# Kernel tuning notes

Hardware: AMD Instinct MI355X
Metric: run time of the kernel (lower is better)

Reference implementation:

```python
import jax, jax.numpy as jnp
import numpy as np
from jax import lax

MARGIN = 0.5
EPS = 1e-12


def _l2norm(x, axis=-1):
    n = jnp.sqrt(jnp.sum(x * x, axis=axis, keepdims=True))
    return x / jnp.maximum(n, EPS)


def setup_inputs() -> dict:
    key = jax.random.key(0)
    ks = jax.random.split(key, 18)
    B, T, N, Din = 1, 8, 4096, 128
    hid = 256
    D = 2 * hid  # out_dim = 2*hidden_dim[-1]
    Tp, Ttr, M, K = 4, 5, 2048, 16
    s = 0.05
    return {
        "x_feature": jax.random.normal(ks[0], (B, Ttr, N, 1), jnp.float32),
        "x_graph": jax.random.normal(ks[1], (B, T, N, Din), jnp.float32),
        "x_graph_inv": jax.random.normal(ks[2], (B, T, N, Din), jnp.float32),
        "temp_y": jax.random.randint(ks[3], (Tp, M, 2 + K), 0, N),
        "is_leaf": jax.random.uniform(ks[4], (Tp, N), dtype=jnp.float32),
        "W_gcn": jax.random.normal(ks[5], (Din, hid), jnp.float32) * s,
        "b_gcn": jnp.zeros((hid,), jnp.float32),
        "Wx_zr": jax.random.normal(ks[6], (D, 2 * D), jnp.float32) * s,
        "Wh_zr": jax.random.normal(ks[7], (D, 2 * D), jnp.float32) * s,
        "b_zr": jnp.zeros((2 * D,), jnp.float32),
        "Wx_c": jax.random.normal(ks[8], (D, D), jnp.float32) * s,
        "Wh_c": jax.random.normal(ks[9], (D, D), jnp.float32) * s,
        "b_c": jnp.zeros((D,), jnp.float32),
        "h_vecs": jax.random.normal(ks[10], (Tp, D), jnp.float32),
        "W_leaf": jax.random.normal(ks[11], (D, 1), jnp.float32) * s,
        "b_leaf": jnp.zeros((1,), jnp.float32),
        "W_conv": jax.random.normal(ks[12], (Ttr, Tp), jnp.float32) * s,
        "b_conv": jnp.zeros((Tp,), jnp.float32),
        "cur_node_num": N,
    }


def reference(x_feature, x_graph, x_graph_inv, temp_y, is_leaf,
              W_gcn, b_gcn, Wx_zr, Wh_zr, b_zr, Wx_c, Wh_c, b_c,
              h_vecs, W_leaf, b_leaf, W_conv, b_conv, cur_node_num):
    B = x_graph.shape[0]
    N_all = x_graph.shape[2]
    # t_gcn on both graph views, concat -> [B,T,N,D]
    h = jax.nn.relu(jnp.einsum('btnd,dh->btnh', x_graph, W_gcn) + b_gcn)
    h_inv = jax.nn.relu(jnp.einsum('btnd,dh->btnh', x_graph_inv, W_gcn) + b_gcn)
    h_final = jnp.concatenate((h, h_inv), axis=-1)
    D = h_final.shape[-1]

    # sequential GRU (TGCNCell) over time_span via scan
    def cell(hs, x):
        zr = jax.nn.sigmoid(x @ Wx_zr + hs @ Wh_zr + b_zr)
        z, r = jnp.split(zr, 2, axis=-1)
        c = jnp.tanh(x @ Wx_c + (r * hs) @ Wh_c + b_c)
        return z * hs + (1.0 - z) * c, None

    h0 = jnp.zeros((B, N_all, D), h_final.dtype)
    hT, _ = lax.scan(cell, h0, jnp.moveaxis(h_final, 1, 0))
    h_trans = _l2norm(hT.reshape(-1, D)[:cur_node_num])  # [N,D]

    # grid predictions (t_conv surrogate): [B,Ttr,N,1] -> [Tp, B*N] -> [Tp,N]
    feat = x_feature[..., 0].transpose(0, 2, 1)            # [B,N,Ttr]
    g = feat @ W_conv + b_conv                             # [B,N,Tp]
    grid_x = jnp.moveaxis(g, 2, 0).reshape(g.shape[-1], -1)[:, :cur_node_num]

    # Householder reflections per predicted step
    hn = _l2norm(h_vecs)                                   # [Tp,D]
    W_trans = jnp.eye(D, dtype=hn.dtype) - 2.0 * hn[:, :, None] * hn[:, None, :]

    leaf_logits = jax.nn.sigmoid(h_trans @ W_leaf + b_leaf)  # [N,1]
    lvec = leaf_logits[:, 0]

    def per_t(W_t, idx_t, yleaf_t, grid_t):
        pos = h_trans[idx_t[:, 1]]            # [M,D]
        neg = h_trans[idx_t[:, 2:]]           # [M,K,D]
        a = pos @ W_t                          # [M,D]
        score_neg = 1.0 - jnp.einsum('md,mkd->mk', a, neg)
        score_pos = 1.0 - jnp.sum(a * pos, axis=-1, keepdims=True)
        loss_off = jnp.mean(jax.nn.relu(score_pos - score_neg + MARGIN))
        # BCEWithLogits applied to sigmoid outputs (faithful to source)
        loss_leaf = jnp.mean(jnp.maximum(lvec, 0.0) - lvec * yleaf_t + jnp.log1p(jnp.exp(-jnp.abs(lvec))))
        h_s = h_trans @ W_t                    # [N,D]
        score_all = h_s @ h_s.T                # [N,N]
        final = lvec * grid_t                  # [N]
        att = score_all @ final                # [N]
        return att, loss_off, loss_leaf

    att_pre, lo, ll = jax.vmap(per_t)(W_trans, temp_y, is_leaf, grid_x)
    return att_pre, jnp.mean(lo), jnp.mean(ll)
```

## Files before the change

kernel.cpp:

```cpp
#include <hip/hip_runtime.h>
#include <hip/hip_bf16.h>
#include <hip/hip_fp16.h>
#include <math.h>

typedef __hip_bfloat16 bf16;
typedef __attribute__((ext_vector_type(8))) short short8;
typedef __attribute__((ext_vector_type(4))) float f32x4;

union UB { short8 v; bf16 e[8]; };
union UH { short8 v; __half e[8]; };

__device__ __forceinline__ float wred(float v) {
  #pragma unroll
  for (int o = 32; o > 0; o >>= 1) v += __shfl_xor(v, o, 64);
  return v;
}
__device__ __forceinline__ float sigf(float x) { return 1.f / (1.f + expf(-x)); }

__device__ __forceinline__ void gl_lds16(const bf16* g, const bf16* lds) {
  __builtin_amdgcn_global_load_lds((const __attribute__((address_space(1))) void*)g,
                                   (__attribute__((address_space(3))) void*)lds,
                                   16, 0, 0);
}
__device__ __forceinline__ f32x4 mfma16(short8 a, short8 b, f32x4 c) {
  return __builtin_amdgcn_mfma_f32_16x16x32_bf16(a, b, c, 0, 0, 0);
}

__global__ __launch_bounds__(256, 2)
void gemmx(const bf16* __restrict__ A, const bf16* __restrict__ Wxzrt,
           const bf16* __restrict__ Wxct, const float* __restrict__ b_zr,
           const float* __restrict__ b_c, bf16* __restrict__ xzrp,
           bf16* __restrict__ xcp)
{
  __shared__ __align__(16) char smem[34816];
  bf16* As = (bf16*)smem;
  bf16* Bs = (bf16*)(smem + 16384);
  __half* Ts = (__half*)smem;

  const int tid  = threadIdx.x;
  const int wave = tid >> 6, lane = tid & 63;
  const int lm = lane & 15, q = lane >> 4;
  const int brow = blockIdx.x, bcol = blockIdx.y;
  const int wr = (wave >> 1) * 64, wc = (wave & 1) * 64;
  const int srow = lane >> 3, sslot = lane & 7;

  const bf16* Bt; const float* bias; bf16* C; int ldc, colbase;
  if (bcol < 8) { Bt = Wxzrt + (size_t)bcol * 128 * 512; bias = b_zr; C = xzrp; ldc = 1024; colbase = bcol * 128; }
  else          { Bt = Wxct + (size_t)(bcol - 8) * 128 * 512; bias = b_c; C = xcp; ldc = 512; colbase = (bcol - 8) * 128; }

  f32x4 acc[4][4];
  #pragma unroll
  for (int i = 0; i < 4; ++i)
    #pragma unroll
    for (int j = 0; j < 4; ++j) acc[i][j] = (f32x4){0.f, 0.f, 0.f, 0.f};

  for (int kb = 0; kb < 512; kb += 64) {
    #pragma unroll
    for (int j = 0; j < 4; ++j) {
      int ml = wave * 32 + j * 8 + srow;
      int cg = sslot ^ (ml & 7);
      gl_lds16(A + (size_t)(brow * 128 + ml) * 512 + kb + cg * 8, As + (wave * 4 + j) * 512);
      gl_lds16(Bt + (size_t)ml * 512 + kb + cg * 8, Bs + (wave * 4 + j) * 512);
    }
    __syncthreads();
    #pragma unroll
    for (int ks = 0; ks < 2; ++ks) {
      short8 af[4], bfr[4];
      #pragma unroll
      for (int i = 0; i < 4; ++i) {
        int cg = ks * 4 + q;
        int ml = wr + i * 16 + lm;
        af[i]  = *(const short8*)(As + ml * 64 + ((cg ^ (ml & 7)) * 8));
        int nl = wc + i * 16 + lm;
        bfr[i] = *(const short8*)(Bs + nl * 64 + ((cg ^ (nl & 7)) * 8));
      }
      #pragma unroll
      for (int i = 0; i < 4; ++i)
        #pragma unroll
        for (int j = 0; j < 4; ++j)
          acc[i][j] = mfma16(af[i], bfr[j], acc[i][j]);
    }
    __syncthreads();
  }
  #pragma unroll
  for (int i = 0; i < 4; ++i)
    #pragma unroll
    for (int j = 0; j < 4; ++j) {
      int col = wc + j * 16 + lm;
      float bv = bias[colbase + col];
      #pragma unroll
      for (int p = 0; p < 4; ++p)
        Ts[(wr + i * 16 + q * 4 + p) * 136 + col] = __float2half(acc[i][j][p] + bv);
    }
  __syncthreads();
  int rg = tid >> 4, cl = tid & 15;
  #pragma unroll
  for (int v = 0; v < 8; ++v) {
    int row = v * 16 + rg;
    UH t; t.v = *(const short8*)(Ts + row * 136 + cl * 8);
    UB o;
    #pragma unroll
    for (int e = 0; e < 8; ++e) o.e[e] = __float2bfloat16(__half2float(t.e[e]));
    *(short8*)(C + (size_t)(brow * 128 + row) * ldc + colbase + cl * 8) = o.v;
  }
}

__global__ __launch_bounds__(256, 2)
void gcnk(const float* __restrict__ Ag, const float* __restrict__ Agi,
          const bf16* __restrict__ Wgt, const float* __restrict__ bias,
          bf16* __restrict__ out)
{
  __shared__ __align__(16) char smem[34816];
  bf16* As = (bf16*)smem;
  bf16* Bs = (bf16*)(smem + 16384);
  __half* Ts = (__half*)smem;

  const int tid  = threadIdx.x;
  const int wave = tid >> 6, lane = tid & 63;
  const int lm = lane & 15, q = lane >> 4;
  const int brow = blockIdx.x, bcol = blockIdx.y;
  const int z = blockIdx.z, cout = z * 256;
  const float* A = z ? Agi : Ag;
  const int wr = (wave >> 1) * 64, wc = (wave & 1) * 64;
  const int srow = lane >> 3, sslot = lane & 7;

  f32x4 acc[4][4];
  #pragma unroll
  for (int i = 0; i < 4; ++i)
    #pragma unroll
    for (int j = 0; j < 4; ++j) acc[i][j] = (f32x4){0.f, 0.f, 0.f, 0.f};

  for (int kb = 0; kb < 128; kb += 64) {
    #pragma unroll
    for (int j = 0; j < 4; ++j) {
      int ml = wave * 32 + j * 8 + srow;
      int cg = sslot ^ (ml & 7);
      const float* src = A + (size_t)(brow * 128 + ml) * 128 + kb + cg * 8;
      bf16 tmp[8];
      #pragma unroll
      for (int e = 0; e < 8; ++e) tmp[e] = __float2bfloat16(src[e]);
      *(short8*)(As + ml * 64 + sslot * 8) = *(const short8*)tmp;
      gl_lds16(Wgt + (size_t)(bcol * 128 + ml) * 128 + kb + cg * 8,
               Bs + (wave * 4 + j) * 512);
    }
    __syncthreads();
    #pragma unroll
    for (int ks = 0; ks < 2; ++ks) {
      short8 af[4], bfr[4];
      #pragma unroll
      for (int i = 0; i < 4; ++i) {
        int cg = ks * 4 + q;
        int ml = wr + i * 16 + lm;
        af[i]  = *(const short8*)(As + ml * 64 + ((cg ^ (ml & 7)) * 8));
        int nl = wc + i * 16 + lm;
        bfr[i] = *(const short8*)(Bs + nl * 64 + ((cg ^ (nl & 7)) * 8));
      }
      #pragma unroll
      for (int i = 0; i < 4; ++i)
        #pragma unroll
        for (int j = 0; j < 4; ++j)
          acc[i][j] = mfma16(af[i], bfr[j], acc[i][j]);
    }
    __syncthreads();
  }
  #pragma unroll
  for (int i = 0; i < 4; ++i)
    #pragma unroll
    for (int j = 0; j < 4; ++j) {
      int col = wc + j * 16 + lm;
      float bv = bias[bcol * 128 + col];
      #pragma unroll
      for (int p = 0; p < 4; ++p)
        Ts[(wr + i * 16 + q * 4 + p) * 136 + col] = __float2half(acc[i][j][p] + bv);
    }
  __syncthreads();
  int rg = tid >> 4, cl = tid & 15;
  #pragma unroll
  for (int v = 0; v < 8; ++v) {
    int row = v * 16 + rg;
    UH t; t.v = *(const short8*)(Ts + row * 136 + cl * 8);
    UB o;
    #pragma unroll
    for (int e = 0; e < 8; ++e) o.e[e] = __float2bfloat16(fmaxf(__half2float(t.e[e]), 0.f));
    *(short8*)(out + (size_t)(brow * 128 + row) * 512 + cout + bcol * 128 + cl * 8) = o.v;
  }
}

__global__ __launch_bounds__(512, 2)
void gruz(const bf16* __restrict__ hsb, const bf16* __restrict__ Wzr,
          const bf16* __restrict__ xz, __half* __restrict__ zh,
          bf16* __restrict__ rhb, int t0)
{
  __shared__ __align__(16) bf16 As[64 * 512];
  __half* Ts = (__half*)As;

  const int tid  = threadIdx.x;
  const int w    = tid >> 6, lane = tid & 63;
  const int lm   = lane & 15, q = lane >> 4;
  const int g    = blockIdx.x, s = blockIdx.y;
  const int grow = g * 64;

  const int prow = tid >> 3, pc0 = (tid & 7) * 32;
  const size_t gr = (size_t)(grow + prow);
  UB xv[4], h8[4];
  #pragma unroll
  for (int j = 0; j < 4; ++j)
    xv[j].v = *(const short8*)(xz + gr * 1024 + s * 256 + pc0 + j * 8);
  if (s >= 2 && !t0) {
    #pragma unroll
    for (int j = 0; j < 4; ++j)
      h8[j].v = *(const short8*)(hsb + gr * 512 + (s - 2) * 256 + pc0 + j * 8);
  }

  f32x4 acc[4][2];
  #pragma unroll
  for (int mf = 0; mf < 4; ++mf)
    #pragma unroll
    for (int nf = 0; nf < 2; ++nf) acc[mf][nf] = (f32x4){0.f, 0.f, 0.f, 0.f};

  if (!t0) {
    #pragma unroll
    for (int j = 0; j < 8; ++j) {
      int row = w * 8 + j;
      gl_lds16(hsb + (size_t)(grow + row) * 512 + ((lane ^ (row & 7)) * 8),
               As + row * 512);
    }
    __syncthreads();

    const bf16* Bp = Wzr + (size_t)(s * 16 + w * 2) * 8192 + lane * 8;
    short8 b0[2], b1[2], a[4];
    #pragma unroll
    for (int nf = 0; nf < 2; ++nf) {
      b0[nf] = *(const short8*)(Bp + (size_t)nf * 8192);
      b1[nf] = *(const short8*)(Bp + (size_t)nf * 8192 + 512);
    }
    #pragma unroll
    for (int mf = 0; mf < 4; ++mf) {
      int row = mf * 16 + lm;
      a[mf] = *(const short8*)(As + row * 512 + ((q ^ (row & 7)) * 8));
    }
    #pragma unroll
    for (int KS = 0; KS < 16; ++KS) {
      short8 bn[2], an[4];
      if (KS < 14) {
        #pragma unroll
        for (int nf = 0; nf < 2; ++nf)
          bn[nf] = *(const short8*)(Bp + (size_t)nf * 8192 + (KS + 2) * 512);
      }
      if (KS < 15) {
        #pragma unroll
        for (int mf = 0; mf < 4; ++mf) {
          int row = mf * 16 + lm;
          an[mf] = *(const short8*)(As + row * 512 + ((((KS + 1) * 4 + q) ^ (row & 7)) * 8));
        }
      }
      #pragma unroll
      for (int nf = 0; nf < 2; ++nf)
        #pragma unroll
        for (int mf = 0; mf < 4; ++mf)
          acc[mf][nf] = mfma16(a[mf], b0[nf], acc[mf][nf]);
      #pragma unroll
      for (int nf = 0; nf < 2; ++nf) { b0[nf] = b1[nf]; b1[nf] = bn[nf]; }
      #pragma unroll
      for (int mf = 0; mf < 4; ++mf) a[mf] = an[mf];
    }
    __syncthreads();
  }

  #pragma unroll
  for (int mf = 0; mf < 4; ++mf)
    #pragma unroll
    for (int nf = 0; nf < 2; ++nf)
      #pragma unroll
      for (int p = 0; p < 4; ++p)
        Ts[(mf * 16 + q * 4 + p) * 264 + w * 32 + nf * 16 + lm] =
          __float2half(acc[mf][nf][p]);
  __syncthreads();

  #pragma unroll
  for (int j = 0; j < 4; ++j) {
    int c = pc0 + j * 8;
    UH tv; tv.v = *(const short8*)(Ts + prow * 264 + c);
    if (s < 2) {
      UH o;
      #pragma unroll
      for (int e = 0; e < 8; ++e)
        o.e[e] = __float2half(sigf(__half2float(tv.e[e]) + (float)xv[j].e[e]));
      *(short8*)(zh + gr * 512 + s * 256 + c) = o.v;
    } else if (!t0) {
      UB o;
      #pragma unroll
      for (int e = 0; e < 8; ++e) {
        float r = sigf(__half2float(tv.e[e]) + (float)xv[j].e[e]);
        o.e[e] = __float2bfloat16(r * (float)h8[j].e[e]);
      }
      *(short8*)(rhb + gr * 512 + (s - 2) * 256 + c) = o.v;
    }
  }
}

__global__ __launch_bounds__(512, 2)
void gruc(const bf16* __restrict__ rhb, const bf16* __restrict__ Wc,
          const bf16* __restrict__ xc, const __half* __restrict__ zh,
          bf16* __restrict__ hsb, int t0)
{
  __shared__ __align__(16) bf16 As[64 * 512];
  __half* Ts = (__half*)As;

  const int tid  = threadIdx.x;
  const int w    = tid >> 6, lane = tid & 63;
  const int lm   = lane & 15, q = lane >> 4;
  const int rh_  = w & 1, cq = w >> 1;
  const int g    = blockIdx.x, s = blockIdx.y;
  const int grow = g * 64;

  const int prow = tid >> 3, pc0 = (tid & 7) * 16;
  const size_t gr = (size_t)(grow + prow);
  UB xv[2], h8[2]; UH zv[2];
  #pragma unroll
  for (int j = 0; j < 2; ++j) {
    int hc = s * 128 + pc0 + j * 8;
    xv[j].v = *(const short8*)(xc + gr * 512 + hc);
    zv[j].v = *(const short8*)(zh + gr * 512 + hc);
  }
  if (!t0) {
    #pragma unroll
    for (int j = 0; j < 2; ++j)
      h8[j].v = *(const short8*)(hsb + gr * 512 + s * 128 + pc0 + j * 8);
  }

  f32x4 acc[2][2];
  #pragma unroll
  for (int mf = 0; mf < 2; ++mf)
    #pragma unroll
    for (int nf = 0; nf < 2; ++nf) acc[mf][nf] = (f32x4){0.f, 0.f, 0.f, 0.f};

  if (!t0) {
    #pragma unroll
    for (int j = 0; j < 8; ++j) {
      int row = w * 8 + j;
      gl_lds16(rhb + (size_t)(grow + row) * 512 + ((lane ^ (row & 7)) * 8),
               As + row * 512);
    }
    __syncthreads();

    const bf16* Bp = Wc + (size_t)(s * 8 + cq * 2) * 8192 + lane * 8;
    short8 b0[2], b1[2], a[2];
    #pragma unroll
    for (int nf = 0; nf < 2; ++nf) {
      b0[nf] = *(const short8*)(Bp + (size_t)nf * 8192);
      b1[nf] = *(const short8*)(Bp + (size_t)nf * 8192 + 512);
    }
    #pragma unroll
    for (int mf = 0; mf < 2; ++mf) {
      int row = rh_ * 32 + mf * 16 + lm;
      a[mf] = *(const short8*)(As + row * 512 + ((q ^ (row & 7)) * 8));
    }
    #pragma unroll
    for (int KS = 0; KS < 16; ++KS) {
      short8 bn[2], an[2];
      if (KS < 14) {
        #pragma unroll
        for (int nf = 0; nf < 2; ++nf)
          bn[nf] = *(const short8*)(Bp + (size_t)nf * 8192 + (KS + 2) * 512);
      }
      if (KS < 15) {
        #pragma unroll
        for (int mf = 0; mf < 2; ++mf) {
          int row = rh_ * 32 + mf * 16 + lm;
          an[mf] = *(const short8*)(As + row * 512 + ((((KS + 1) * 4 + q) ^ (row & 7)) * 8));
        }
      }
      #pragma unroll
      for (int nf = 0; nf < 2; ++nf)
        #pragma unroll
        for (int mf = 0; mf < 2; ++mf)
          acc[mf][nf] = mfma16(a[mf], b0[nf], acc[mf][nf]);
      #pragma unroll
      for (int nf = 0; nf < 2; ++nf) { b0[nf] = b1[nf]; b1[nf] = bn[nf]; }
      #pragma unroll
      for (int mf = 0; mf < 2; ++mf) a[mf] = an[mf];
    }
    __syncthreads();
  }

  #pragma unroll
  for (int mf = 0; mf < 2; ++mf)
    #pragma unroll
    for (int nf = 0; nf < 2; ++nf)
      #pragma unroll
      for (int p = 0; p < 4; ++p)
        Ts[(rh_ * 32 + mf * 16 + q * 4 + p) * 136 + cq * 32 + nf * 16 + lm] =
          __float2half(acc[mf][nf][p]);
  __syncthreads();

  #pragma unroll
  for (int j = 0; j < 2; ++j) {
    int c = pc0 + j * 8;
    int hc = s * 128 + c;
    UH tv; tv.v = *(const short8*)(Ts + prow * 136 + c);
    UB o;
    #pragma unroll
    for (int e = 0; e < 8; ++e) {
      float cd = tanhf(__half2float(tv.e[e]) + (float)xv[j].e[e]);
      float zc = __half2float(zv[j].e[e]);
      float ho = t0 ? 0.f : (float)h8[j].e[e];
      o.e[e] = __float2bfloat16(zc * ho + (1.f - zc) * cd);
    }
    *(short8*)(hsb + gr * 512 + hc) = o.v;
  }
}

__global__ void prep(const float* __restrict__ Wh_zr, const float* __restrict__ Wh_c,
                     const float* __restrict__ Wx_zr, const float* __restrict__ Wx_c,
                     const float* __restrict__ W_gcn,
                     bf16* __restrict__ Whzrt, bf16* __restrict__ Whct,
                     bf16* __restrict__ Wxzrt, bf16* __restrict__ Wxct,
                     bf16* __restrict__ Wgt) {
  int i = blockIdx.x * 256 + threadIdx.x;
  if (i < 524288) {
    int n = i >> 9, k = i & 511;
    int off = ((n >> 4) * 16 + (k >> 5)) * 512 + ((k >> 3) & 3) * 128 + (n & 15) * 8 + (k & 7);
    Whzrt[off] = __float2bfloat16(Wh_zr[(size_t)k * 1024 + n]);
  } else if (i < 786432) {
    int j = i - 524288; int n = j >> 9, k = j & 511;
    int off = ((n >> 4) * 16 + (k >> 5)) * 512 + ((k >> 3) & 3) * 128 + (n & 15) * 8 + (k & 7);
    Whct[off] = __float2bfloat16(Wh_c[(size_t)k * 512 + n]);
  } else if (i < 1310720) {
    int j = i - 786432; int n = j >> 9, k = j & 511;
    Wxzrt[j] = __float2bfloat16(Wx_zr[(size_t)k * 1024 + n]);
  } else if (i < 1572864) {
    int j = i - 1310720; int n = j >> 9, k = j & 511;
    Wxct[j] = __float2bfloat16(Wx_c[(size_t)k * 512 + n]);
  } else {
    int j = i - 1572864; int n = j >> 7, k = j & 127;
    Wgt[j] = __float2bfloat16(W_gcn[(size_t)k * 256 + n]);
  }
}

__global__ void norm_lvec(const bf16* __restrict__ hsb, const float* __restrict__ Wl,
                          const float* __restrict__ bl, const float* __restrict__ hv,
                          bf16* __restrict__ Htrb, float* __restrict__ lv,
                          float* __restrict__ hn) {
  int w = threadIdx.x >> 6, lane = threadIdx.x & 63;
  if (blockIdx.x == 1024) {
    float x[8], ss = 0.f;
    #pragma unroll
    for (int j = 0; j < 8; ++j) { x[j] = hv[w * 512 + lane * 8 + j]; ss += x[j] * x[j]; }
    ss = wred(ss);
    float inv = 1.f / fmaxf(sqrtf(ss), 1e-12f);
    #pragma unroll
    for (int j = 0; j < 8; ++j) hn[w * 512 + lane * 8 + j] = x[j] * inv;
    return;
  }
  int n = blockIdx.x * 4 + w;
  float x[8], ss = 0.f;
  #pragma unroll
  for (int j = 0; j < 8; ++j) {
    x[j] = (float)hsb[(size_t)n * 512 + lane * 8 + j];
    ss += x[j] * x[j];
  }
  ss = wred(ss);
  float inv = 1.f / fmaxf(sqrtf(ss), 1e-12f);
  float dot = 0.f;
  #pragma unroll
  for (int j = 0; j < 8; ++j) {
    float vv = x[j] * inv;
    Htrb[(size_t)n * 512 + lane * 8 + j] = __float2bfloat16(vv);
    dot += vv * Wl[lane * 8 + j];
  }
  dot = wred(dot);
  if (lane == 0) lv[n] = sigf(dot + bl[0]);
}

__global__ void htf(const bf16* __restrict__ Htrb, const float* __restrict__ xf,
                    const float* __restrict__ Wc, const float* __restrict__ bc,
                    const float* __restrict__ lv, float* __restrict__ v) {
  __shared__ float fin_s[4][64];
  int ch = blockIdx.x;
  int d = threadIdx.x;
  int n0 = ch * 64;
  if (d < 256) {
    int t = d >> 6, i = d & 63, n = n0 + i;
    float g = bc[t];
    #pragma unroll
    for (int tt = 0; tt < 5; ++tt) g += xf[tt * 4096 + n] * Wc[tt * 4 + t];
    fin_s[t][i] = lv[n] * g;
  }
  __syncthreads();
  float s0 = 0.f, s1 = 0.f, s2 = 0.f, s3 = 0.f;
  for (int i = 0; i < 64; ++i) {
    float hv = (float)Htrb[(size_t)(n0 + i) * 512 + d];
    s0 += hv * fin_s[0][i];
    s1 += hv * fin_s[1][i];
    s2 += hv * fin_s[2][i];
    s3 += hv * fin_s[3][i];
  }
  atomicAdd(&v[d], s0);
  atomicAdd(&v[512 + d], s1);
  atomicAdd(&v[1024 + d], s2);
  atomicAdd(&v[1536 + d], s3);
}

__global__ void attk(const bf16* __restrict__ Htrb, const float* __restrict__ v,
                     float* __restrict__ out) {
  int w = threadIdx.x >> 6, lane = threadIdx.x & 63;
  int n = blockIdx.x * 4 + w;
  float x[8];
  #pragma unroll
  for (int j = 0; j < 8; ++j) x[j] = (float)Htrb[(size_t)n * 512 + lane * 8 + j];
  #pragma unroll
  for (int t = 0; t < 4; ++t) {
    float s = 0.f;
    #pragma unroll
    for (int j = 0; j < 8; ++j) s += x[j] * v[t * 512 + lane * 8 + j];
    s = wred(s);
    if (lane == 0) out[t * 4096 + n] = s;
  }
}

__global__ void loff(const bf16* __restrict__ Htrb, const float* __restrict__ hn,
                     const int* __restrict__ ty, float* __restrict__ loffp) {
  int w = threadIdx.x >> 6, lane = threadIdx.x & 63;
  int t = blockIdx.y;
  int m = blockIdx.x * 4 + w;
  const int* row = ty + ((size_t)t * 2048 + m) * 18;
  int pi = row[1];
  float p[8], hv[8], c = 0.f;
  #pragma unroll
  for (int j = 0; j < 8; ++j) {
    p[j]  = (float)Htrb[(size_t)pi * 512 + lane * 8 + j];
    hv[j] = hn[t * 512 + lane * 8 + j];
    c += p[j] * hv[j];
  }
  c = wred(c);
  float a[8], sp = 0.f;
  #pragma unroll
  for (int j = 0; j < 8; ++j) { a[j] = p[j] - 2.f * c * hv[j]; sp += a[j] * p[j]; }
  sp = wred(sp);
  float acc = 0.f;
  for (int k = 0; k < 16; ++k) {
    int ni = row[2 + k];
    float sn = 0.f;
    #pragma unroll
    for (int j = 0; j < 8; ++j) sn += a[j] * (float)Htrb[(size_t)ni * 512 + lane * 8 + j];
    sn = wred(sn);
    acc += fmaxf(sn - sp + 0.5f, 0.f);
  }
  __shared__ float sbuf[4];
  if (lane == 0) sbuf[w] = acc;
  __syncthreads();
  if (threadIdx.x == 0)
    loffp[t * 512 + blockIdx.x] = sbuf[0] + sbuf[1] + sbuf[2] + sbuf[3];
}

__global__ void fini(const float* __restrict__ loffp, const float* __restrict__ lv,
                     const float* __restrict__ yl, float* __restrict__ out) {
  int tid = threadIdx.x, w = tid >> 6, lane = tid & 63;
  float s = 0.f, s2 = 0.f;
  for (int i = tid; i < 2048; i += 256) s += loffp[i];
  for (int i = tid; i < 4096; i += 256) {
    float l = lv[i];
    float ym = 0.25f * (yl[i] + yl[4096 + i] + yl[8192 + i] + yl[12288 + i]);
    s2 += fmaxf(l, 0.f) - l * ym + log1pf(expf(-fabsf(l)));
  }
  s = wred(s); s2 = wred(s2);
  __shared__ float sb[4], sb2[4];
  if (lane == 0) { sb[w] = s; sb2[w] = s2; }
  __syncthreads();
  if (tid == 0) {
    out[16384] = (sb[0] + sb[1] + sb[2] + sb[3]) / (4.f * 2048.f * 16.f);
    out[16385] = (sb2[0] + sb2[1] + sb2[2] + sb2[3]) / 4096.f;
  }
}

__global__ void wsprobe(float marker, float* out) {
  if (threadIdx.x == 0) out[0] = marker;
}

extern "C" void kernel_launch(void* const* d_in, const int* in_sizes, int n_in,
                              void* d_out, int out_size, void* d_ws, size_t ws_size,
                              hipStream_t stream) {
  const float* x_feature   = (const float*)d_in[0];
  const float* x_graph     = (const float*)d_in[1];
  const float* x_graph_inv = (const float*)d_in[2];
  const int*   temp_y      = (const int*)d_in[3];
  const float* is_leaf     = (const float*)d_in[4];
  const float* W_gcn       = (const float*)d_in[5];
  const float* b_gcn       = (const float*)d_in[6];
  const float* Wx_zr       = (const float*)d_in[7];
  const float* Wh_zr       = (const float*)d_in[8];
  const float* b_zr        = (const float*)d_in[9];
  const float* Wx_c        = (const float*)d_in[10];
  const float* Wh_c        = (const float*)d_in[11];
  const float* b_c         = (const float*)d_in[12];
  const float* h_vecs      = (const float*)d_in[13];
  const float* W_leaf      = (const float*)d_in[14];
  const float* b_leaf      = (const float*)d_in[15];
  const float* W_conv      = (const float*)d_in[16];
  const float* b_conv      = (const float*)d_in[17];
  float* out = (float*)d_out;
  (void)in_sizes; (void)n_in; (void)out_size;

  const size_t NEED = 156000000;
  if (ws_size < NEED) {
    wsprobe<<<1, 64, 0, stream>>>(1000.f + (float)(ws_size >> 20), out);
    return;
  }

  char* ws = (char*)d_ws;
  size_t off = 0;
  auto alloc = [&](size_t bytes) -> void* {
    void* p = ws + off;
    off = (off + bytes + 255) & ~(size_t)255;
    return p;
  };
  bf16*   Whzrt = (bf16*)  alloc((size_t)1024 * 512 * 2);
  bf16*   Whct  = (bf16*)  alloc((size_t)512 * 512 * 2);
  bf16*   Wxzrt = (bf16*)  alloc((size_t)1024 * 512 * 2);
  bf16*   Wxct  = (bf16*)  alloc((size_t)512 * 512 * 2);
  bf16*   Wgt   = (bf16*)  alloc((size_t)256 * 128 * 2);
  bf16*   hfin  = (bf16*)  alloc((size_t)32768 * 512 * 2);
  bf16*   xzrp  = (bf16*)  alloc((size_t)32768 * 1024 * 2);
  bf16*   xcp   = (bf16*)  alloc((size_t)32768 * 512 * 2);
  bf16*   hsb   = (bf16*)  alloc((size_t)4096 * 512 * 2);
  bf16*   rhb   = (bf16*)  alloc((size_t)4096 * 512 * 2);
  __half* zh    = (__half*)alloc((size_t)4096 * 512 * 2);
  float*  lv    = (float*) alloc(4096 * 4);
  float*  hn    = (float*) alloc(4 * 512 * 4);
  float*  v     = (float*) alloc(4 * 512 * 4);
  float*  loffp = (float*) alloc(2048 * 4);
  bf16*   Htrb  = hfin;

  hipMemsetAsync(v, 0, 4 * 512 * 4, stream);

  prep<<<6272, 256, 0, stream>>>(Wh_zr, Wh_c, Wx_zr, Wx_c, W_gcn,
                                 Whzrt, Whct, Wxzrt, Wxct, Wgt);
  gcnk<<<dim3(256, 2, 2), 256, 0, stream>>>(x_graph, x_graph_inv, Wgt, b_gcn, hfin);
  gemmx<<<dim3(256, 12), 256, 0, stream>>>(hfin, Wxzrt, Wxct, b_zr, b_c, xzrp, xcp);

  for (int t = 0; t < 8; ++t) {
    gruz<<<dim3(64, 4), 512, 0, stream>>>(hsb, Whzrt,
                                          xzrp + (size_t)t * 4096 * 1024,
                                          zh, rhb, t == 0);
    gruc<<<dim3(64, 4), 512, 0, stream>>>(rhb, Whct,
                                          xcp + (size_t)t * 4096 * 512,
                                          zh, hsb, t == 0);
  }

  norm_lvec<<<1025, 256, 0, stream>>>(hsb, W_leaf, b_leaf, h_vecs, Htrb, lv, hn);
  htf<<<64, 512, 0, stream>>>(Htrb, x_feature, W_conv, b_conv, lv, v);
  attk<<<1024, 256, 0, stream>>>(Htrb, v, out);
  loff<<<dim3(512, 4), 256, 0, stream>>>(Htrb, hn, temp_y, loffp);
  fini<<<1, 256, 0, stream>>>(loffp, lv, is_leaf, out);
}
```

Before: 423.8 us.

## Fuse GRU time loop into one persistent kernel with per-group spin barriers

Replaces the 16 separate gruz/gruc launches across 8 timesteps with a single persistent kernel of 256 blocks. Groups of 4 blocks that share a 64-row slice synchronise through atomic counters in global memory, and hsb/rhb are loaded with a cache-coherent flag. This removes launch overhead and the device-wide kernel boundaries between recurrent steps. The cost is that correctness depends on all 256 blocks being resident at once, which is needed to avoid deadlock, and the spin-waiting adds its own overhead.

```diff
diff --git a/kernel.cpp b/kernel.cpp
--- a/kernel.cpp
+++ b/kernel.cpp
@@ -22,8 +22,27 @@
                                    (__attribute__((address_space(3))) void*)lds,
                                    16, 0, 0);
 }
+__device__ __forceinline__ void gl_lds16c(const bf16* g, const bf16* lds) {
+  __builtin_amdgcn_global_load_lds((const __attribute__((address_space(1))) void*)g,
+                                   (__attribute__((address_space(3))) void*)lds,
+                                   16, 0, 1);
+}
 __device__ __forceinline__ f32x4 mfma16(short8 a, short8 b, f32x4 c) {
   return __builtin_amdgcn_mfma_f32_16x16x32_bf16(a, b, c, 0, 0, 0);
+}
+
+__device__ __forceinline__ void gang_sync(unsigned* f) {
+  __syncthreads();
+  if (threadIdx.x == 0) {
+    __hip_atomic_fetch_add(f, 1u, __ATOMIC_RELEASE, __HIP_MEMORY_SCOPE_AGENT);
+    int it = 0;
+    while (__hip_atomic_load(f, __ATOMIC_RELAXED, __HIP_MEMORY_SCOPE_AGENT) < 4u) {
+      __builtin_amdgcn_s_sleep(2);
+      if (++it > (1 << 27)) break;
+    }
+    (void)__hip_atomic_load(f, __ATOMIC_ACQUIRE, __HIP_MEMORY_SCOPE_AGENT);
+  }
+  __syncthreads();
 }
 
 __global__ __launch_bounds__(256, 2)
@@ -187,9 +206,10 @@
 }
 
 __global__ __launch_bounds__(512, 2)
-void gruz(const bf16* __restrict__ hsb, const bf16* __restrict__ Wzr,
-          const bf16* __restrict__ xz, __half* __restrict__ zh,
-          bf16* __restrict__ rhb, int t0)
+void grup(const bf16* __restrict__ Wzr, const bf16* __restrict__ Wc,
+          const bf16* __restrict__ xzrp, const bf16* __restrict__ xcp,
+          __half* __restrict__ zh, bf16* __restrict__ rhb,
+          bf16* __restrict__ hsb, unsigned* __restrict__ flags)
 {
   __shared__ __align__(16) bf16 As[64 * 512];
   __half* Ts = (__half*)As;
@@ -197,217 +217,217 @@
   const int tid  = threadIdx.x;
   const int w    = tid >> 6, lane = tid & 63;
   const int lm   = lane & 15, q = lane >> 4;
-  const int g    = blockIdx.x, s = blockIdx.y;
+  const int bid  = blockIdx.x;
+  const int s    = (bid >> 3) & 3;
+  const int g    = ((bid >> 5) << 3) | (bid & 7);
   const int grow = g * 64;
-
-  const int prow = tid >> 3, pc0 = (tid & 7) * 32;
+  const int rh_  = w & 1, cq = w >> 1;
+  const int prow = tid >> 3;
   const size_t gr = (size_t)(grow + prow);
-  UB xv[4], h8[4];
-  #pragma unroll
-  for (int j = 0; j < 4; ++j)
-    xv[j].v = *(const short8*)(xz + gr * 1024 + s * 256 + pc0 + j * 8);
-  if (s >= 2 && !t0) {
-    #pragma unroll
-    for (int j = 0; j < 4; ++j)
-      h8[j].v = *(const short8*)(hsb + gr * 512 + (s - 2) * 256 + pc0 + j * 8);
-  }
-
-  f32x4 acc[4][2];
-  #pragma unroll
-  for (int mf = 0; mf < 4; ++mf)
-    #pragma unroll
-    for (int nf = 0; nf < 2; ++nf) acc[mf][nf] = (f32x4){0.f, 0.f, 0.f, 0.f};
-
-  if (!t0) {
-    #pragma unroll
-    for (int j = 0; j < 8; ++j) {
-      int row = w * 8 + j;
-      gl_lds16(hsb + (size_t)(grow + row) * 512 + ((lane ^ (row & 7)) * 8),
-               As + row * 512);
-    }
-    __syncthreads();
-
-    const bf16* Bp = Wzr + (size_t)(s * 16 + w * 2) * 8192 + lane * 8;
-    short8 b0[2], b1[2], a[4];
-    #pragma unroll
-    for (int nf = 0; nf < 2; ++nf) {
-      b0[nf] = *(const short8*)(Bp + (size_t)nf * 8192);
-      b1[nf] = *(const short8*)(Bp + (size_t)nf * 8192 + 512);
-    }
-    #pragma unroll
-    for (int mf = 0; mf < 4; ++mf) {
-      int row = mf * 16 + lm;
-      a[mf] = *(const short8*)(As + row * 512 + ((q ^ (row & 7)) * 8));
-    }
-    #pragma unroll
-    for (int KS = 0; KS < 16; ++KS) {
-      short8 bn[2], an[4];
-      if (KS < 14) {
-        #pragma unroll
-        for (int nf = 0; nf < 2; ++nf)
-          bn[nf] = *(const short8*)(Bp + (size_t)nf * 8192 + (KS + 2) * 512);
-      }
-      if (KS < 15) {
+  const int pc1 = (tid & 7) * 32;
+  const int pc2 = (tid & 7) * 16;
+  unsigned* gf = flags + g * 16;
+
+  for (int t = 0; t < 8; ++t) {
+    const bool t0 = (t == 0);
+    const bf16* xz = xzrp + (size_t)t * 4096 * 1024;
+    const bf16* xc = xcp  + (size_t)t * 4096 * 512;
+
+    {
+      UB xv[4], h8[4];
+      #pragma unroll
+      for (int j = 0; j < 4; ++j)
+        xv[j].v = *(const short8*)(xz + gr * 1024 + s * 256 + pc1 + j * 8);
+      if (s >= 2 && !t0) {
+        #pragma unroll
+        for (int j = 0; j < 4; ++j)
+          h8[j].v = *(const short8*)(hsb + gr * 512 + (s - 2) * 256 + pc1 + j * 8);
+      }
+
+      f32x4 acc[4][2];
+      #pragma unroll
+      for (int mf = 0; mf < 4; ++mf)
+        #pragma unroll
+        for (int nf = 0; nf < 2; ++nf) acc[mf][nf] = (f32x4){0.f, 0.f, 0.f, 0.f};
+
+      if (!t0) {
+        #pragma unroll
+        for (int j = 0; j < 8; ++j) {
+          int row = w * 8 + j;
+          gl_lds16c(hsb + (size_t)(grow + row) * 512 + ((lane ^ (row & 7)) * 8),
+                    As + row * 512);
+        }
+        __syncthreads();
+
+        const bf16* Bp = Wzr + (size_t)(s * 16 + w * 2) * 8192 + lane * 8;
+        short8 b0[2], b1[2], a[4];
+        #pragma unroll
+        for (int nf = 0; nf < 2; ++nf) {
+          b0[nf] = *(const short8*)(Bp + (size_t)nf * 8192);
+          b1[nf] = *(const short8*)(Bp + (size_t)nf * 8192 + 512);
+        }
         #pragma unroll
         for (int mf = 0; mf < 4; ++mf) {
           int row = mf * 16 + lm;
-          an[mf] = *(const short8*)(As + row * 512 + ((((KS + 1) * 4 + q) ^ (row & 7)) * 8));
-        }
-      }
-      #pragma unroll
-      for (int nf = 0; nf < 2; ++nf)
-        #pragma unroll
-        for (int mf = 0; mf < 4; ++mf)
-          acc[mf][nf] = mfma16(a[mf], b0[nf], acc[mf][nf]);
-      #pragma unroll
-      for (int nf = 0; nf < 2; ++nf) { b0[nf] = b1[nf]; b1[nf] = bn[nf]; }
-      #pragma unroll
-      for (int mf = 0; mf < 4; ++mf) a[mf] = an[mf];
-    }
-    __syncthreads();
-  }
-
-  #pragma unroll
-  for (int mf = 0; mf < 4; ++mf)
-    #pragma unroll
-    for (int nf = 0; nf < 2; ++nf)
-      #pragma unroll
-      for (int p = 0; p < 4; ++p)
-        Ts[(mf * 16 + q * 4 + p) * 264 + w * 32 + nf * 16 + lm] =
-          __float2half(acc[mf][nf][p]);
-  __syncthreads();
-
-  #pragma unroll
-  for (int j = 0; j < 4; ++j) {
-    int c = pc0 + j * 8;
-    UH tv; tv.v = *(const short8*)(Ts + prow * 264 + c);
-    if (s < 2) {
-      UH o;
-      #pragma unroll
-      for (int e = 0; e < 8; ++e)
-        o.e[e] = __float2half(sigf(__half2float(tv.e[e]) + (float)xv[j].e[e]));
-      *(short8*)(zh + gr * 512 + s * 256 + c) = o.v;
-    } else if (!t0) {
-      UB o;
-      #pragma unroll
-      for (int e = 0; e < 8; ++e) {
-        float r = sigf(__half2float(tv.e[e]) + (float)xv[j].e[e]);
-        o.e[e] = __float2bfloat16(r * (float)h8[j].e[e]);
-      }
-      *(short8*)(rhb + gr * 512 + (s - 2) * 256 + c) = o.v;
-    }
-  }
-}
-
-__global__ __launch_bounds__(512, 2)
-void gruc(const bf16* __restrict__ rhb, const bf16* __restrict__ Wc,
-          const bf16* __restrict__ xc, const __half* __restrict__ zh,
-          bf16* __restrict__ hsb, int t0)
-{
-  __shared__ __align__(16) bf16 As[64 * 512];
-  __half* Ts = (__half*)As;
-
-  const int tid  = threadIdx.x;
-  const int w    = tid >> 6, lane = tid & 63;
-  const int lm   = lane & 15, q = lane >> 4;
-  const int rh_  = w & 1, cq = w >> 1;
-  const int g    = blockIdx.x, s = blockIdx.y;
-  const int grow = g * 64;
-
-  const int prow = tid >> 3, pc0 = (tid & 7) * 16;
-  const size_t gr = (size_t)(grow + prow);
-  UB xv[2], h8[2]; UH zv[2];
-  #pragma unroll
-  for (int j = 0; j < 2; ++j) {
-    int hc = s * 128 + pc0 + j * 8;
-    xv[j].v = *(const short8*)(xc + gr * 512 + hc);
-    zv[j].v = *(const short8*)(zh + gr * 512 + hc);
-  }
-  if (!t0) {
-    #pragma unroll
-    for (int j = 0; j < 2; ++j)
-      h8[j].v = *(const short8*)(hsb + gr * 512 + s * 128 + pc0 + j * 8);
-  }
-
-  f32x4 acc[2][2];
-  #pragma unroll
-  for (int mf = 0; mf < 2; ++mf)
-    #pragma unroll
-    for (int nf = 0; nf < 2; ++nf) acc[mf][nf] = (f32x4){0.f, 0.f, 0.f, 0.f};
-
-  if (!t0) {
-    #pragma unroll
-    for (int j = 0; j < 8; ++j) {
-      int row = w * 8 + j;
-      gl_lds16(rhb + (size_t)(grow + row) * 512 + ((lane ^ (row & 7)) * 8),
-               As + row * 512);
-    }
-    __syncthreads();
-
-    const bf16* Bp = Wc + (size_t)(s * 8 + cq * 2) * 8192 + lane * 8;
-    short8 b0[2], b1[2], a[2];
-    #pragma unroll
-    for (int nf = 0; nf < 2; ++nf) {
-      b0[nf] = *(const short8*)(Bp + (size_t)nf * 8192);
-      b1[nf] = *(const short8*)(Bp + (size_t)nf * 8192 + 512);
-    }
-    #pragma unroll
-    for (int mf = 0; mf < 2; ++mf) {
-      int row = rh_ * 32 + mf * 16 + lm;
-      a[mf] = *(const short8*)(As + row * 512 + ((q ^ (row & 7)) * 8));
-    }
-    #pragma unroll
-    for (int KS = 0; KS < 16; ++KS) {
-      short8 bn[2], an[2];
-      if (KS < 14) {
+          a[mf] = *(const short8*)(As + row * 512 + ((q ^ (row & 7)) * 8));
+        }
+        #pragma unroll
+        for (int KS = 0; KS < 16; ++KS) {
+          short8 bn[2], an[4];
+          if (KS < 14) {
+            #pragma unroll
+            for (int nf = 0; nf < 2; ++nf)
+              bn[nf] = *(const short8*)(Bp + (size_t)nf * 8192 + (KS + 2) * 512);
+          }
+          if (KS < 15) {
+            #pragma unroll
+            for (int mf = 0; mf < 4; ++mf) {
+              int row = mf * 16 + lm;
+              an[mf] = *(const short8*)(As + row * 512 + ((((KS + 1) * 4 + q) ^ (row & 7)) * 8));
+            }
+          }
+          #pragma unroll
+          for (int nf = 0; nf < 2; ++nf)
+            #pragma unroll
+            for (int mf = 0; mf < 4; ++mf)
+              acc[mf][nf] = mfma16(a[mf], b0[nf], acc[mf][nf]);
+          #pragma unroll
+          for (int nf = 0; nf < 2; ++nf) { b0[nf] = b1[nf]; b1[nf] = bn[nf]; }
+          #pragma unroll
+          for (int mf = 0; mf < 4; ++mf) a[mf] = an[mf];
+        }
+        __syncthreads();
+      }
+
+      #pragma unroll
+      for (int mf = 0; mf < 4; ++mf)
         #pragma unroll
         for (int nf = 0; nf < 2; ++nf)
-          bn[nf] = *(const short8*)(Bp + (size_t)nf * 8192 + (KS + 2) * 512);
-      }
-      if (KS < 15) {
+          #pragma unroll
+          for (int p = 0; p < 4; ++p)
+            Ts[(mf * 16 + q * 4 + p) * 264 + w * 32 + nf * 16 + lm] =
+              __float2half(acc[mf][nf][p]);
+      __syncthreads();
+
+      #pragma unroll
+      for (int j = 0; j < 4; ++j) {
+        int c = pc1 + j * 8;
+        UH tv; tv.v = *(const short8*)(Ts + prow * 264 + c);
+        if (s < 2) {
+          UH o;
+          #pragma unroll
+          for (int e = 0; e < 8; ++e)
+            o.e[e] = __float2half(sigf(__half2float(tv.e[e]) + (float)xv[j].e[e]));
+          *(short8*)(zh + gr * 512 + s * 256 + c) = o.v;
+        } else if (!t0) {
+          UB o;
+          #pragma unroll
+          for (int e = 0; e < 8; ++e) {
+            float r = sigf(__half2float(tv.e[e]) + (float)xv[j].e[e]);
+            o.e[e] = __float2bfloat16(r * (float)h8[j].e[e]);
+          }
+          *(short8*)(rhb + gr * 512 + (s - 2) * 256 + c) = o.v;
+        }
+      }
+    }
+    gang_sync(gf + 2 * t);
+
+    {
+      UB xv[2], h8[2]; UH zv[2];
+      #pragma unroll
+      for (int j = 0; j < 2; ++j) {
+        int hc = s * 128 + pc2 + j * 8;
+        xv[j].v = *(const short8*)(xc + gr * 512 + hc);
+        zv[j].v = *(const short8*)(zh + gr * 512 + hc);
+      }
+      if (!t0) {
+        #pragma unroll
+        for (int j = 0; j < 2; ++j)
+          h8[j].v = *(const short8*)(hsb + gr * 512 + s * 128 + pc2 + j * 8);
+      }
+
+      f32x4 acc[2][2];
+      #pragma unroll
+      for (int mf = 0; mf < 2; ++mf)
+        #pragma unroll
+        for (int nf = 0; nf < 2; ++nf) acc[mf][nf] = (f32x4){0.f, 0.f, 0.f, 0.f};
+
+      if (!t0) {
+        #pragma unroll
+        for (int j = 0; j < 8; ++j) {
+          int row = w * 8 + j;
+          gl_lds16c(rhb + (size_t)(grow + row) * 512 + ((lane ^ (row & 7)) * 8),
+                    As + row * 512);
+        }
+        __syncthreads();
+
+        const bf16* Bp = Wc + (size_t)(s * 8 + cq * 2) * 8192 + lane * 8;
+        short8 b0[2], b1[2], a[2];
+        #pragma unroll
+        for (int nf = 0; nf < 2; ++nf) {
+          b0[nf] = *(const short8*)(Bp + (size_t)nf * 8192);
+          b1[nf] = *(const short8*)(Bp + (size_t)nf * 8192 + 512);
+        }
         #pragma unroll
         for (int mf = 0; mf < 2; ++mf) {
           int row = rh_ * 32 + mf * 16 + lm;
-          an[mf] = *(const short8*)(As + row * 512 + ((((KS + 1) * 4 + q) ^ (row & 7)) * 8));
-        }
-      }
-      #pragma unroll
-      for (int nf = 0; nf < 2; ++nf)
-        #pragma unroll
-        for (int mf = 0; mf < 2; ++mf)
-          acc[mf][nf] = mfma16(a[mf], b0[nf], acc[mf][nf]);
-      #pragma unroll
-      for (int nf = 0; nf < 2; ++nf) { b0[nf] = b1[nf]; b1[nf] = bn[nf]; }
-      #pragma unroll
-      for (int mf = 0; mf < 2; ++mf) a[mf] = an[mf];
-    }
-    __syncthreads();
-  }
-
-  #pragma unroll
-  for (int mf = 0; mf < 2; ++mf)
-    #pragma unroll
-    for (int nf = 0; nf < 2; ++nf)
-      #pragma unroll
-      for (int p = 0; p < 4; ++p)
-        Ts[(rh_ * 32 + mf * 16 + q * 4 + p) * 136 + cq * 32 + nf * 16 + lm] =
-          __float2half(acc[mf][nf][p]);
-  __syncthreads();
-
-  #pragma unroll
-  for (int j = 0; j < 2; ++j) {
-    int c = pc0 + j * 8;
-    int hc = s * 128 + c;
-    UH tv; tv.v = *(const short8*)(Ts + prow * 136 + c);
-    UB o;
-    #pragma unroll
-    for (int e = 0; e < 8; ++e) {
-      float cd = tanhf(__half2float(tv.e[e]) + (float)xv[j].e[e]);
-      float zc = __half2float(zv[j].e[e]);
-      float ho = t0 ? 0.f : (float)h8[j].e[e];
-      o.e[e] = __float2bfloat16(zc * ho + (1.f - zc) * cd);
-    }
-    *(short8*)(hsb + gr * 512 + hc) = o.v;
+          a[mf] = *(const short8*)(As + row * 512 + ((q ^ (row & 7)) * 8));
+        }
+        #pragma unroll
+        for (int KS = 0; KS < 16; ++KS) {
+          short8 bn[2], an[2];
+          if (KS < 14) {
+            #pragma unroll
+            for (int nf = 0; nf < 2; ++nf)
+              bn[nf] = *(const short8*)(Bp + (size_t)nf * 8192 + (KS + 2) * 512);
+          }
+          if (KS < 15) {
+            #pragma unroll
+            for (int mf = 0; mf < 2; ++mf) {
+              int row = rh_ * 32 + mf * 16 + lm;
+              an[mf] = *(const short8*)(As + row * 512 + ((((KS + 1) * 4 + q) ^ (row & 7)) * 8));
+            }
+          }
+          #pragma unroll
+          for (int nf = 0; nf < 2; ++nf)
+            #pragma unroll
+            for (int mf = 0; mf < 2; ++mf)
+              acc[mf][nf] = mfma16(a[mf], b0[nf], acc[mf][nf]);
+          #pragma unroll
+          for (int nf = 0; nf < 2; ++nf) { b0[nf] = b1[nf]; b1[nf] = bn[nf]; }
+          #pragma unroll
+          for (int mf = 0; mf < 2; ++mf) a[mf] = an[mf];
+        }
+        __syncthreads();
+      }
+
+      #pragma unroll
+      for (int mf = 0; mf < 2; ++mf)
+        #pragma unroll
+        for (int nf = 0; nf < 2; ++nf)
+          #pragma unroll
+          for (int p = 0; p < 4; ++p)
+            Ts[(rh_ * 32 + mf * 16 + q * 4 + p) * 136 + cq * 32 + nf * 16 + lm] =
+              __float2half(acc[mf][nf][p]);
+      __syncthreads();
+
+      #pragma unroll
+      for (int j = 0; j < 2; ++j) {
+        int c = pc2 + j * 8;
+        int hc = s * 128 + c;
+        UH tv; tv.v = *(const short8*)(Ts + prow * 136 + c);
+        UB o;
+        #pragma unroll
+        for (int e = 0; e < 8; ++e) {
+          float cd = tanhf(__half2float(tv.e[e]) + (float)xv[j].e[e]);
+          float zc = __half2float(zv[j].e[e]);
+          float ho = t0 ? 0.f : (float)h8[j].e[e];
+          o.e[e] = __float2bfloat16(zc * ho + (1.f - zc) * cd);
+        }
+        *(short8*)(hsb + gr * 512 + hc) = o.v;
+      }
+    }
+    if (t < 7) gang_sync(gf + 2 * t + 1);
   }
 }
 
@@ -630,23 +650,18 @@
   float*  hn    = (float*) alloc(4 * 512 * 4);
   float*  v     = (float*) alloc(4 * 512 * 4);
   float*  loffp = (float*) alloc(2048 * 4);
+  unsigned* flags = (unsigned*)alloc(64 * 16 * 4);
   bf16*   Htrb  = hfin;
 
   hipMemsetAsync(v, 0, 4 * 512 * 4, stream);
+  hipMemsetAsync(flags, 0, 64 * 16 * 4, stream);
 
   prep<<<6272, 256, 0, stream>>>(Wh_zr, Wh_c, Wx_zr, Wx_c, W_gcn,
                                  Whzrt, Whct, Wxzrt, Wxct, Wgt);
   gcnk<<<dim3(256, 2, 2), 256, 0, stream>>>(x_graph, x_graph_inv, Wgt, b_gcn, hfin);
   gemmx<<<dim3(256, 12), 256, 0, stream>>>(hfin, Wxzrt, Wxct, b_zr, b_c, xzrp, xcp);
 
-  for (int t = 0; t < 8; ++t) {
-    gruz<<<dim3(64, 4), 512, 0, stream>>>(hsb, Whzrt,
-                                          xzrp + (size_t)t * 4096 * 1024,
-                                          zh, rhb, t == 0);
-    gruc<<<dim3(64, 4), 512, 0, stream>>>(rhb, Whct,
-                                          xcp + (size_t)t * 4096 * 512,
-                                          zh, hsb, t == 0);
-  }
+  grup<<<256, 512, 0, stream>>>(Whzrt, Whct, xzrp, xcp, zh, rhb, hsb, flags);
 
   norm_lvec<<<1025, 256, 0, stream>>>(hsb, W_leaf, b_leaf, h_vecs, Htrb, lv, hn);
   htf<<<64, 512, 0, stream>>>(Htrb, x_feature, W_conv, b_conv, lv, v);
```

New measurement: 610.3 us. 44.0% more time.
